# Kernel tuning notes

Hardware: AMD Instinct MI355X
Metric: run time of the kernel (lower is better)

Reference implementation:

```python
import jax, jax.numpy as jnp
import numpy as np

# Static problem sizes (must match input construction)
B, G, EPG, K, C = 64, 24, 512, 20, 1
NS = B * G            # total number of subgraphs
E = NS * EPG          # total number of edges
M, H = 4096, 256      # node_state shape


def setup_inputs() -> dict:
    key = jax.random.key(0)
    ks = jax.random.split(key, 8)
    label = (jax.random.uniform(ks[0], (E,)) < 0.5).astype(jnp.float32)
    label0 = (jax.random.uniform(ks[1], (E,)) < 0.5).astype(jnp.float32)
    log_theta = jax.random.normal(ks[2], (E, K), dtype=jnp.float32)
    log_theta0 = jax.random.normal(ks[3], (E, K), dtype=jnp.float32)
    log_alpha = jax.random.normal(ks[4], (E, K), dtype=jnp.float32)
    log_alpha0 = jax.random.normal(ks[5], (E, K), dtype=jnp.float32)
    subgraph_idx = (jnp.arange(E, dtype=jnp.int32) // EPG).astype(jnp.int32)
    subgraph_idx0 = subgraph_idx
    subgraph_idx_base = (jnp.arange(B + 1, dtype=jnp.int32) * (G * C)).astype(jnp.int32)
    subgraph_idx_base0 = subgraph_idx_base
    node_state = jax.random.normal(ks[6], (M, H), dtype=jnp.float32)
    node_state0 = jax.random.normal(ks[7], (M, H), dtype=jnp.float32)
    return {
        "label": label, "label0": label0,
        "log_theta": log_theta, "log_theta0": log_theta0,
        "log_alpha": log_alpha, "log_alpha0": log_alpha0,
        "subgraph_idx": subgraph_idx, "subgraph_idx0": subgraph_idx0,
        "subgraph_idx_base": subgraph_idx_base, "subgraph_idx_base0": subgraph_idx_base0,
        "node_state": node_state, "node_state0": node_state0,
    }


def _bce_with_logits(logits, y):
    # BCEWithLogitsLoss(reduction='none'), broadcast label over K mixture components
    return -(y[:, None] * jax.nn.log_sigmoid(logits)
             + (1.0 - y)[:, None] * jax.nn.log_sigmoid(-logits))


def _stream_loss(label, log_theta, log_alpha, subgraph_idx, subgraph_idx_base):
    adj_loss = _bce_with_logits(log_theta, label)                     # E x K
    const = jax.ops.segment_sum(jnp.ones((E,), jnp.float32), subgraph_idx, NS)  # edges per subgraph
    reduce_adj_loss = jax.ops.segment_sum(adj_loss, subgraph_idx, NS)  # NS x K
    reduce_log_alpha = jax.ops.segment_sum(log_alpha, subgraph_idx, NS) / const[:, None]
    reduce_log_alpha = jax.nn.log_softmax(reduce_log_alpha, axis=-1)
    log_prob = jax.nn.logsumexp(-reduce_adj_loss + reduce_log_alpha, axis=1)  # NS
    # bc_idx: map each subgraph to its (batch, canonical-order) slot; C == 1 here,
    # equivalent to repeat_interleave(arange(B*C), bc_size) in the original.
    bc_idx = jnp.searchsorted(subgraph_idx_base, jnp.arange(NS, dtype=jnp.int32), side='right') - 1
    bc_log_prob = jax.ops.segment_sum(log_prob, bc_idx, B * C).reshape(B, C)
    bc_const = jax.ops.segment_sum(const, bc_idx, B * C).reshape(B, C)
    bc_loss = bc_log_prob / bc_const
    b_loss = jax.nn.logsumexp(bc_loss, axis=1)   # sum_order_log_prob=False
    return jnp.mean(-b_loss)                      # reduction='mean'


def _trace_cdist(ns, ns0):
    # Fused replacement for the naive O(m^2) host-side pairwise-distance loop:
    # D[i,j] = ||ns[i] - ns0[j]||, then trace(D).
    x2 = jnp.sum(ns * ns, axis=1)
    y2 = jnp.sum(ns0 * ns0, axis=1)
    d2 = x2[:, None] + y2[None, :] - 2.0 * (ns @ ns0.T)   # M x M
    D = jnp.sqrt(jnp.maximum(d2, 0.0))
    return jnp.trace(D)


def reference(label, label0, log_theta, log_theta0, log_alpha, log_alpha0,
              subgraph_idx, subgraph_idx0, subgraph_idx_base, subgraph_idx_base0,
              node_state, node_state0):
    loss = _stream_loss(label, log_theta, log_alpha, subgraph_idx, subgraph_idx_base)
    loss0 = _stream_loss(label0, log_theta0, log_alpha0, subgraph_idx0, subgraph_idx_base0)
    trD = _trace_cdist(node_state, node_state0)
    # return_neg_log_prob=False branch of the original
    return 10.0 * (loss + loss0) + trD
```

## Files before the change

### kernel.cpp

```cpp
#include <hip/hip_runtime.h>
#include <math.h>

#define B_   64
#define G_   24
#define EPG_ 512
#define K_   20
#define NS_  (B_ * G_)
#define E_   (NS_ * EPG_)
#define M_   4096
#define H_   256

#define NT_  320
#define F4_  (EPG_ * K_ / 4)
#define IT_  (F4_ / NT_)

__global__ __launch_bounds__(NT_)
void stream_loss_kernel(const float* __restrict__ label,
                        const float* __restrict__ label0,
                        const float* __restrict__ log_theta,
                        const float* __restrict__ log_theta0,
                        const float* __restrict__ log_alpha,
                        const float* __restrict__ log_alpha0,
                        float* __restrict__ out)
{
    const int s   = blockIdx.x;
    const int tid = threadIdx.x;

    const float* lab = (blockIdx.y == 0) ? label     : label0;
    const float4* lt4 = (const float4*)((blockIdx.y == 0) ? log_theta : log_theta0);
    const float4* la4 = (const float4*)((blockIdx.y == 0) ? log_alpha : log_alpha0);

    __shared__ float  s_label[EPG_];
    __shared__ float4 red_adj[NT_];
    __shared__ float4 red_alpha[NT_];
    __shared__ float  S_adj[K_];
    __shared__ float  S_alpha[K_];

    {
        const float4* labp4 = (const float4*)(lab + (size_t)s * EPG_);
        if (tid < EPG_ / 4) ((float4*)s_label)[tid] = labp4[tid];
    }
    __syncthreads();

    const int e_div = tid / 5;

    float4 acc_adj   = make_float4(0.f, 0.f, 0.f, 0.f);
    float4 acc_alpha = make_float4(0.f, 0.f, 0.f, 0.f);

    const size_t base4 = (size_t)s * F4_;
    #pragma unroll
    for (int i = 0; i < IT_; ++i) {
        const float y = s_label[i * 64 + e_div];
        const size_t f = base4 + (size_t)i * NT_ + tid;
        const float4 x = lt4[f];
        const float4 a = la4[f];
        acc_adj.x += fmaxf(x.x, 0.f) - x.x * y + __logf(1.f + __expf(-fabsf(x.x)));
        acc_adj.y += fmaxf(x.y, 0.f) - x.y * y + __logf(1.f + __expf(-fabsf(x.y)));
        acc_adj.z += fmaxf(x.z, 0.f) - x.z * y + __logf(1.f + __expf(-fabsf(x.z)));
        acc_adj.w += fmaxf(x.w, 0.f) - x.w * y + __logf(1.f + __expf(-fabsf(x.w)));
        acc_alpha.x += a.x;
        acc_alpha.y += a.y;
        acc_alpha.z += a.z;
        acc_alpha.w += a.w;
    }
    red_adj[tid]   = acc_adj;
    red_alpha[tid] = acc_alpha;
    __syncthreads();

    if (tid < K_) {
        const int q = tid >> 2;
        const int j = tid & 3;
        float sa = 0.0f, sl = 0.0f;
        #pragma unroll
        for (int m = 0; m < 64; ++m) {
            const int t = m * 5 + q;
            sa += ((const float*)&red_adj[t])[j];
            sl += ((const float*)&red_alpha[t])[j];
        }
        S_adj[tid]   = sa;
        S_alpha[tid] = sl;
    }
    __syncthreads();

    if (tid == 0) {
        const float inv_const = 1.0f / (float)EPG_;
        float m1 = -INFINITY;
        #pragma unroll
        for (int i = 0; i < K_; ++i) m1 = fmaxf(m1, S_alpha[i] * inv_const);
        float sum1 = 0.0f;
        #pragma unroll
        for (int i = 0; i < K_; ++i) sum1 += __expf(S_alpha[i] * inv_const - m1);
        const float lse = m1 + __logf(sum1);

        float m2 = -INFINITY;
        #pragma unroll
        for (int i = 0; i < K_; ++i) {
            const float v = -S_adj[i] + S_alpha[i] * inv_const - lse;
            m2 = fmaxf(m2, v);
        }
        float sum2 = 0.0f;
        #pragma unroll
        for (int i = 0; i < K_; ++i) {
            const float v = -S_adj[i] + S_alpha[i] * inv_const - lse;
            sum2 += __expf(v - m2);
        }
        const float lp = m2 + __logf(sum2);

        atomicAdd(out, lp * (-10.0f / (float)E_));
    }
}

__global__ __launch_bounds__(256)
void trace_cdist_kernel(const float* __restrict__ ns,
                        const float* __restrict__ ns0,
                        float* __restrict__ out)
{
    const int wave = threadIdx.x >> 6;
    const int lane = threadIdx.x & 63;
    __shared__ float s_d[16];

    #pragma unroll
    for (int i = 0; i < 4; ++i) {
        const int row = blockIdx.x * 16 + wave * 4 + i;
        const float4* a = (const float4*)(ns  + (size_t)row * H_);
        const float4* b = (const float4*)(ns0 + (size_t)row * H_);
        const float4 av = a[lane];
        const float4 bv = b[lane];
        const float dx = av.x - bv.x;
        const float dy = av.y - bv.y;
        const float dz = av.z - bv.z;
        const float dw = av.w - bv.w;
        float sv = dx * dx + dy * dy + dz * dz + dw * dw;
        #pragma unroll
        for (int off = 32; off > 0; off >>= 1) sv += __shfl_down(sv, off);
        if (lane == 0) s_d[wave * 4 + i] = sqrtf(sv);
    }
    __syncthreads();
    if (threadIdx.x == 0) {
        float t = 0.0f;
        #pragma unroll
        for (int i = 0; i < 16; ++i) t += s_d[i];
        atomicAdd(out, t);
    }
}

extern "C" void kernel_launch(void* const* d_in, const int* in_sizes, int n_in,
                              void* d_out, int out_size, void* d_ws, size_t ws_size,
                              hipStream_t stream) {
    const float* label       = (const float*)d_in[0];
    const float* label0      = (const float*)d_in[1];
    const float* log_theta   = (const float*)d_in[2];
    const float* log_theta0  = (const float*)d_in[3];
    const float* log_alpha   = (const float*)d_in[4];
    const float* log_alpha0  = (const float*)d_in[5];
    const float* node_state  = (const float*)d_in[10];
    const float* node_state0 = (const float*)d_in[11];
    float* out = (float*)d_out;

    hipMemsetAsync(out, 0, sizeof(float), stream);

    dim3 grid(NS_, 2);
    stream_loss_kernel<<<grid, NT_, 0, stream>>>(label, label0,
                                                 log_theta, log_theta0,
                                                 log_alpha, log_alpha0, out);
    trace_cdist_kernel<<<M_ / 16, 256, 0, stream>>>(node_state, node_state0, out);
}
```

Before: 267.5 us.

## Fuse trace-cdist and both loss streams into one kernel with prefetching

Merges the trace-distance kernel and the stream-loss kernel into a single launch. The first blocks handle the cdist rows (20 rows per 320-thread block) and the rest each process one subgraph for both streams at once. The main loop software-prefetches the next iteration's four float4 loads. The final per-K reduction is spread across many threads with shuffles, replacing the single-thread serial sum. The aim is to remove launch overhead and add memory-level parallelism, at the cost of more registers and a larger shared-memory footprint per block.

```diff
diff --git a/kernel.cpp b/kernel.cpp
--- a/kernel.cpp
+++ b/kernel.cpp
@@ -14,134 +14,146 @@
 #define F4_  (EPG_ * K_ / 4)
 #define IT_  (F4_ / NT_)
 
-__global__ __launch_bounds__(NT_)
-void stream_loss_kernel(const float* __restrict__ label,
-                        const float* __restrict__ label0,
-                        const float* __restrict__ log_theta,
-                        const float* __restrict__ log_theta0,
-                        const float* __restrict__ log_alpha,
-                        const float* __restrict__ log_alpha0,
-                        float* __restrict__ out)
+#define CD_ROWS_   20
+#define CD_BLOCKS_ ((M_ + CD_ROWS_ - 1) / CD_ROWS_)
+
+__device__ __forceinline__ float bce_f(float x, float y) {
+    return fmaxf(x, 0.f) - x * y + __logf(1.f + __expf(-fabsf(x)));
+}
+
+__global__ __launch_bounds__(NT_, 8)
+void fused_kernel(const float* __restrict__ label,
+                  const float* __restrict__ label0,
+                  const float* __restrict__ log_theta,
+                  const float* __restrict__ log_theta0,
+                  const float* __restrict__ log_alpha,
+                  const float* __restrict__ log_alpha0,
+                  const float* __restrict__ ns,
+                  const float* __restrict__ ns0,
+                  float* __restrict__ out)
 {
-    const int s   = blockIdx.x;
+    __shared__ float  s_lab[2][EPG_];
+    __shared__ float4 red_adj[2][NT_];
+    __shared__ float4 red_alpha[2][NT_];
+    __shared__ float  S_red[2][2][K_];
+    __shared__ float  s_lp[2];
+    __shared__ float  s_cd[5];
+
     const int tid = threadIdx.x;
 
-    const float* lab = (blockIdx.y == 0) ? label     : label0;
-    const float4* lt4 = (const float4*)((blockIdx.y == 0) ? log_theta : log_theta0);
-    const float4* la4 = (const float4*)((blockIdx.y == 0) ? log_alpha : log_alpha0);
+    if (blockIdx.x < CD_BLOCKS_) {
+        const int wave = tid >> 6, lane = tid & 63;
+        float acc = 0.f;
+        #pragma unroll
+        for (int i = 0; i < 4; ++i) {
+            const int row = blockIdx.x * CD_ROWS_ + wave * 4 + i;
+            if (row < M_) {
+                const float4 a = ((const float4*)(ns  + (size_t)row * H_))[lane];
+                const float4 b = ((const float4*)(ns0 + (size_t)row * H_))[lane];
+                const float dx = a.x - b.x, dy = a.y - b.y;
+                const float dz = a.z - b.z, dw = a.w - b.w;
+                float sv = dx * dx + dy * dy + dz * dz + dw * dw;
+                #pragma unroll
+                for (int off = 32; off > 0; off >>= 1) sv += __shfl_down(sv, off);
+                if (lane == 0) acc += sqrtf(sv);
+            }
+        }
+        if (lane == 0) s_cd[wave] = acc;
+        __syncthreads();
+        if (tid == 0)
+            atomicAdd(out, s_cd[0] + s_cd[1] + s_cd[2] + s_cd[3] + s_cd[4]);
+        return;
+    }
 
-    __shared__ float  s_label[EPG_];
-    __shared__ float4 red_adj[NT_];
-    __shared__ float4 red_alpha[NT_];
-    __shared__ float  S_adj[K_];
-    __shared__ float  S_alpha[K_];
+    const int s = blockIdx.x - CD_BLOCKS_;
+
+    const float4* t0 = (const float4*)log_theta  + (size_t)s * F4_;
+    const float4* t1 = (const float4*)log_theta0 + (size_t)s * F4_;
+    const float4* a0 = (const float4*)log_alpha  + (size_t)s * F4_;
+    const float4* a1 = (const float4*)log_alpha0 + (size_t)s * F4_;
+
+    float4 lv;
+    if (tid < 128)      lv = ((const float4*)(label  + (size_t)s * EPG_))[tid];
+    else if (tid < 256) lv = ((const float4*)(label0 + (size_t)s * EPG_))[tid - 128];
+
+    float4 cx0 = t0[tid], cx1 = t1[tid], ca0 = a0[tid], ca1 = a1[tid];
+
+    if (tid < 128)      ((float4*)&s_lab[0][0])[tid]       = lv;
+    else if (tid < 256) ((float4*)&s_lab[1][0])[tid - 128] = lv;
+    __syncthreads();
+
+    const int e_div = tid / 5;
+    float4 AJ0 = {0,0,0,0}, AJ1 = {0,0,0,0}, AL0 = {0,0,0,0}, AL1 = {0,0,0,0};
+
+    #pragma unroll
+    for (int i = 0; i < IT_; ++i) {
+        float4 nx0 = cx0, nx1 = cx1, na0 = ca0, na1 = ca1;
+        if (i + 1 < IT_) {
+            const int f = (i + 1) * NT_ + tid;
+            nx0 = t0[f]; nx1 = t1[f]; na0 = a0[f]; na1 = a1[f];
+        }
+        const float y0 = s_lab[0][i * 64 + e_div];
+        const float y1 = s_lab[1][i * 64 + e_div];
+        AJ0.x += bce_f(cx0.x, y0); AJ0.y += bce_f(cx0.y, y0);
+        AJ0.z += bce_f(cx0.z, y0); AJ0.w += bce_f(cx0.w, y0);
+        AJ1.x += bce_f(cx1.x, y1); AJ1.y += bce_f(cx1.y, y1);
+        AJ1.z += bce_f(cx1.z, y1); AJ1.w += bce_f(cx1.w, y1);
+        AL0.x += ca0.x; AL0.y += ca0.y; AL0.z += ca0.z; AL0.w += ca0.w;
+        AL1.x += ca1.x; AL1.y += ca1.y; AL1.z += ca1.z; AL1.w += ca1.w;
+        cx0 = nx0; cx1 = nx1; ca0 = na0; ca1 = na1;
+    }
+
+    red_adj[0][tid]   = AJ0;  red_adj[1][tid]   = AJ1;
+    red_alpha[0][tid] = AL0;  red_alpha[1][tid] = AL1;
+    __syncthreads();
 
     {
-        const float4* labp4 = (const float4*)(lab + (size_t)s * EPG_);
-        if (tid < EPG_ / 4) ((float4*)s_label)[tid] = labp4[tid];
+        const int g = tid >> 2, sub = tid & 3;
+        const int st = g / 40, r = g % 40, which = r / 20, k = r % 20;
+        const int q = k >> 2, j = k & 3;
+        const float* basep = which ? (const float*)&red_alpha[st][0]
+                                   : (const float*)&red_adj[st][0];
+        float v = 0.f;
+        #pragma unroll
+        for (int mm = 0; mm < 16; ++mm) {
+            const int t = (sub * 16 + mm) * 5 + q;
+            v += basep[t * 4 + j];
+        }
+        v += __shfl_down(v, 2);
+        v += __shfl_down(v, 1);
+        if (sub == 0) S_red[st][which][k] = v;
     }
     __syncthreads();
 
-    const int e_div = tid / 5;
+    if (tid == 0 || tid == 64) {
+        const int st = tid >> 6;
+        const float inv_c = 1.0f / (float)EPG_;
+        float va[K_];
+        #pragma unroll
+        for (int k = 0; k < K_; ++k) va[k] = S_red[st][1][k] * inv_c;
+        float m1 = -INFINITY;
+        #pragma unroll
+        for (int k = 0; k < K_; ++k) m1 = fmaxf(m1, va[k]);
+        float s1 = 0.f;
+        #pragma unroll
+        for (int k = 0; k < K_; ++k) s1 += __expf(va[k] - m1);
+        const float lse = m1 + __logf(s1);
 
-    float4 acc_adj   = make_float4(0.f, 0.f, 0.f, 0.f);
-    float4 acc_alpha = make_float4(0.f, 0.f, 0.f, 0.f);
-
-    const size_t base4 = (size_t)s * F4_;
-    #pragma unroll
-    for (int i = 0; i < IT_; ++i) {
-        const float y = s_label[i * 64 + e_div];
-        const size_t f = base4 + (size_t)i * NT_ + tid;
-        const float4 x = lt4[f];
-        const float4 a = la4[f];
-        acc_adj.x += fmaxf(x.x, 0.f) - x.x * y + __logf(1.f + __expf(-fabsf(x.x)));
-        acc_adj.y += fmaxf(x.y, 0.f) - x.y * y + __logf(1.f + __expf(-fabsf(x.y)));
-        acc_adj.z += fmaxf(x.z, 0.f) - x.z * y + __logf(1.f + __expf(-fabsf(x.z)));
-        acc_adj.w += fmaxf(x.w, 0.f) - x.w * y + __logf(1.f + __expf(-fabsf(x.w)));
-        acc_alpha.x += a.x;
-        acc_alpha.y += a.y;
-        acc_alpha.z += a.z;
-        acc_alpha.w += a.w;
-    }
-    red_adj[tid]   = acc_adj;
-    red_alpha[tid] = acc_alpha;
-    __syncthreads();
-
-    if (tid < K_) {
-        const int q = tid >> 2;
-        const int j = tid & 3;
-        float sa = 0.0f, sl = 0.0f;
+        float w[K_];
+        float m2 = -INFINITY;
         #pragma unroll
-        for (int m = 0; m < 64; ++m) {
-            const int t = m * 5 + q;
-            sa += ((const float*)&red_adj[t])[j];
-            sl += ((const float*)&red_alpha[t])[j];
+        for (int k = 0; k < K_; ++k) {
+            w[k] = va[k] - lse - S_red[st][0][k];
+            m2 = fmaxf(m2, w[k]);
         }
-        S_adj[tid]   = sa;
-        S_alpha[tid] = sl;
+        float s2 = 0.f;
+        #pragma unroll
+        for (int k = 0; k < K_; ++k) s2 += __expf(w[k] - m2);
+        s_lp[st] = m2 + __logf(s2);
     }
     __syncthreads();
-
-    if (tid == 0) {
-        const float inv_const = 1.0f / (float)EPG_;
-        float m1 = -INFINITY;
-        #pragma unroll
-        for (int i = 0; i < K_; ++i) m1 = fmaxf(m1, S_alpha[i] * inv_const);
-        float sum1 = 0.0f;
-        #pragma unroll
-        for (int i = 0; i < K_; ++i) sum1 += __expf(S_alpha[i] * inv_const - m1);
-        const float lse = m1 + __logf(sum1);
-
-        float m2 = -INFINITY;
-        #pragma unroll
-        for (int i = 0; i < K_; ++i) {
-            const float v = -S_adj[i] + S_alpha[i] * inv_const - lse;
-            m2 = fmaxf(m2, v);
-        }
-        float sum2 = 0.0f;
-        #pragma unroll
-        for (int i = 0; i < K_; ++i) {
-            const float v = -S_adj[i] + S_alpha[i] * inv_const - lse;
-            sum2 += __expf(v - m2);
-        }
-        const float lp = m2 + __logf(sum2);
-
-        atomicAdd(out, lp * (-10.0f / (float)E_));
-    }
-}
-
-__global__ __launch_bounds__(256)
-void trace_cdist_kernel(const float* __restrict__ ns,
-                        const float* __restrict__ ns0,
-                        float* __restrict__ out)
-{
-    const int wave = threadIdx.x >> 6;
-    const int lane = threadIdx.x & 63;
-    __shared__ float s_d[16];
-
-    #pragma unroll
-    for (int i = 0; i < 4; ++i) {
-        const int row = blockIdx.x * 16 + wave * 4 + i;
-        const float4* a = (const float4*)(ns  + (size_t)row * H_);
-        const float4* b = (const float4*)(ns0 + (size_t)row * H_);
-        const float4 av = a[lane];
-        const float4 bv = b[lane];
-        const float dx = av.x - bv.x;
-        const float dy = av.y - bv.y;
-        const float dz = av.z - bv.z;
-        const float dw = av.w - bv.w;
-        float sv = dx * dx + dy * dy + dz * dz + dw * dw;
-        #pragma unroll
-        for (int off = 32; off > 0; off >>= 1) sv += __shfl_down(sv, off);
-        if (lane == 0) s_d[wave * 4 + i] = sqrtf(sv);
-    }
-    __syncthreads();
-    if (threadIdx.x == 0) {
-        float t = 0.0f;
-        #pragma unroll
-        for (int i = 0; i < 16; ++i) t += s_d[i];
-        atomicAdd(out, t);
-    }
+    if (tid == 0)
+        atomicAdd(out, (s_lp[0] + s_lp[1]) * (-10.0f / (float)E_));
 }
 
 extern "C" void kernel_launch(void* const* d_in, const int* in_sizes, int n_in,
@@ -159,9 +171,7 @@
 
     hipMemsetAsync(out, 0, sizeof(float), stream);
 
-    dim3 grid(NS_, 2);
-    stream_loss_kernel<<<grid, NT_, 0, stream>>>(label, label0,
-                                                 log_theta, log_theta0,
-                                                 log_alpha, log_alpha0, out);
-    trace_cdist_kernel<<<M_ / 16, 256, 0, stream>>>(node_state, node_state0, out);
+    fused_kernel<<<dim3(CD_BLOCKS_ + NS_), NT_, 0, stream>>>(
+        label, label0, log_theta, log_theta0, log_alpha, log_alpha0,
+        node_state, node_state0, out);
 }
```

New measurement: 283.9 us. 6.1% more time.
